# Kernel optimization log

Hardware: AMD Instinct MI355X
Metric: run time of the kernel (lower is better)

The kernel has to match this reference:

```python
import jax, jax.numpy as jnp
import numpy as np

DEPTH = 3
HEADS = 8
DIM = 512
MLP = 4096
NUM_CLASS = 4
EPS = 1e-5
SCALE = (DIM // HEADS) ** -0.5


def _layernorm(x, g, b):
    mu = jnp.mean(x, axis=-1, keepdims=True)
    var = jnp.mean(jnp.square(x - mu), axis=-1, keepdims=True)
    return (x - mu) * jax.lax.rsqrt(var + EPS) * g + b


def setup_inputs() -> dict:
    key = jax.random.key(0)
    ks = jax.random.split(key, 16)
    B, N = 2, 2560
    s = 0.02
    inp = {
        "x": jax.random.normal(ks[0], (B, N, DIM), jnp.float32),
        "mask": jax.random.randint(ks[1], (B, NUM_CLASS), 0, 2, jnp.int32),
        # per-layer params stacked on leading depth axis
        "ln1_g": jnp.ones((DEPTH, DIM), jnp.float32),
        "ln1_b": jnp.zeros((DEPTH, DIM), jnp.float32),
        "qkv_w": jax.random.normal(ks[2], (DEPTH, DIM, 3 * DIM), jnp.float32) * s,  # qkv_bias=False
        "proj_w": jax.random.normal(ks[3], (DEPTH, DIM, DIM), jnp.float32) * s,
        "proj_b": jnp.zeros((DEPTH, DIM), jnp.float32),
        "ln2_g": jnp.ones((DEPTH, DIM), jnp.float32),
        "ln2_b": jnp.zeros((DEPTH, DIM), jnp.float32),
        "ffn_w1": jax.random.normal(ks[4], (DEPTH, DIM, MLP), jnp.float32) * s,
        "ffn_b1": jnp.zeros((DEPTH, MLP), jnp.float32),
        "ffn_w2": jax.random.normal(ks[5], (DEPTH, MLP, DIM), jnp.float32) * s,
        "ffn_b2": jnp.zeros((DEPTH, DIM), jnp.float32),
    }
    return inp


def reference(x, mask, ln1_g, ln1_b, qkv_w, proj_w, proj_b, ln2_g, ln2_b,
              ffn_w1, ffn_b1, ffn_w2, ffn_b2):
    B, N, C = x.shape
    n = N // (NUM_CLASS + 1)  # tokens per modality block
    # mask_gen_fusion: columns of missing-modality blocks are masked out;
    # fusion block (last n tokens) is always attendable.
    avail = jnp.concatenate(
        [jnp.repeat(mask.astype(bool), n, axis=1), jnp.ones((B, n), bool)], axis=1)  # [B, N]
    neg_inf = jnp.asarray(-jnp.inf, x.dtype)

    attn_list = []
    for j in range(DEPTH):
        # --- masked attention block (Residual(PreNormDrop(MaskedAttention))) ---
        h = _layernorm(x, ln1_g[j], ln1_b[j])
        qkv = (h @ qkv_w[j]).reshape(B, N, 3, HEADS, C // HEADS)
        q, k, v = (qkv[:, :, i].transpose(0, 2, 1, 3) for i in range(3))  # [B,H,N,hd]
        attn = jnp.einsum("bhqd,bhkd->bhqk", q, k) * SCALE
        attn = jnp.where(avail[:, None, None, :], attn, neg_inf)
        attn = jax.nn.softmax(attn, axis=-1)
        o = jnp.einsum("bhqk,bhkd->bhqd", attn, v).transpose(0, 2, 1, 3).reshape(B, N, C)
        x = x + (o @ proj_w[j] + proj_b[j])  # dropout = identity (eval)
        attn_list.append(attn)
        # --- FFN block (Residual(PreNorm(FeedForward))) ---
        h = _layernorm(x, ln2_g[j], ln2_b[j])
        h = jax.nn.gelu(h @ ffn_w1[j] + ffn_b1[j]) @ ffn_w2[j] + ffn_b2[j]
        x = x + h
    return x, jnp.stack(attn_list, axis=0)  # [depth,B,H,N,N]
```

## Files before the change

kernel.cpp:

```cpp
#include <hip/hip_runtime.h>
#include <math.h>

#define DEPTH 3
#define HEADS 8
#define DIM 512
#define NCLS 4
#define EPSV 1e-5f
#define BB 2
#define NN 2560
#define HD 64
#define ATT_SCALE 0.125f

typedef __attribute__((ext_vector_type(8))) short bf16x8;
typedef __attribute__((ext_vector_type(4))) float f32x4;

__device__ inline unsigned short bf16_rne(float f) {
    unsigned int u = __float_as_uint(f);
    u += 0x7FFFu + ((u >> 16) & 1u);
    return (unsigned short)(u >> 16);
}
__device__ inline float bf16_tof(unsigned short h) {
    return __uint_as_float(((unsigned int)h) << 16);
}
__device__ inline void split2(float f, unsigned short& hi, unsigned short& lo) {
    hi = bf16_rne(f);
    lo = bf16_rne(f - bf16_tof(hi));
}

__device__ inline float gelu_tanh(float x) {
    float x3 = x * x * x;
    return 0.5f * x * (1.f + tanhf(0.7978845608028654f * (x + 0.044715f * x3)));
}

__device__ inline void gll16(const void* g, void* l) {
    __builtin_amdgcn_global_load_lds(
        (const __attribute__((address_space(1))) void*)g,
        (__attribute__((address_space(3))) void*)l,
        16, 0, 0);
}

template<int ROWS>
__device__ inline void stage_plane(const unsigned short* gp, int ldp,
                                   unsigned short* ls, int lane, int wave) {
#pragma unroll
    for (int q = 0; q < ROWS / 64; ++q) {
        int base = wave * (ROWS * 16) + q * 1024;
        int lpos = base + lane * 16;
        int row  = lpos >> 6;
        int ke   = (lpos & 63) >> 1;
        gll16(gp + (size_t)row * ldp + ke, (char*)ls + base);
    }
}

__device__ inline void stage_a_f32(const float* ga, int lda,
                                   unsigned short* lhi, unsigned short* llo, int tid) {
    int row = tid >> 1, half = tid & 1;
    const float* src = ga + (size_t)row * lda + half * 16;
#pragma unroll
    for (int c2 = 0; c2 < 2; ++c2) {
        float4 p0 = *(const float4*)(src + c2 * 8);
        float4 p1 = *(const float4*)(src + c2 * 8 + 4);
        float v[8] = {p0.x, p0.y, p0.z, p0.w, p1.x, p1.y, p1.z, p1.w};
        bf16x8 hv, lv;
#pragma unroll
        for (int i = 0; i < 8; ++i) {
            unsigned short h, l;
            split2(v[i], h, l);
            hv[i] = (short)h; lv[i] = (short)l;
        }
        int idx = row * 32 + (half * 2 + c2) * 8;
        *(bf16x8*)&lhi[idx] = hv;
        *(bf16x8*)&llo[idx] = lv;
    }
}

template<int BN, bool A_F32, bool DO_GELU, bool DO_RESID, bool SPLIT_OUT>
__global__ __launch_bounds__(256, 2) void gemm_mfma(
    const float* __restrict__ Af,
    const unsigned short* __restrict__ A_hi, const unsigned short* __restrict__ A_lo,
    int lda, long long sAb, long long sAh,
    const unsigned short* __restrict__ B_hi, const unsigned short* __restrict__ B_lo,
    int ldb, long long sBb, long long sBh,
    float* __restrict__ Cf,
    unsigned short* __restrict__ C_hi, unsigned short* __restrict__ C_lo,
    int ldc, long long sCb, long long sCh,
    int K, float alpha, const float* __restrict__ bias, int nh)
{
    constexpr int BM = 128;
    constexpr int WAVES_N = (BN == 128) ? 2 : 1;
    constexpr int WM = (WAVES_N == 2) ? 64 : 32;
    constexpr int WN = 64;
    constexpr int MF = WM / 16;
    constexpr int NF = WN / 16;

    __shared__ unsigned short As_hi[BM * 32], As_lo[BM * 32];
    __shared__ unsigned short Bs_hi[BN * 32], Bs_lo[BN * 32];

    const int bz = blockIdx.z / nh, hz = blockIdx.z % nh;
    const long long aoff = (long long)bz * sAb + (long long)hz * sAh;
    const long long boff = (long long)bz * sBb + (long long)hz * sBh;
    const long long coff = (long long)bz * sCb + (long long)hz * sCh;
    if (A_F32) { Af += aoff; } else { A_hi += aoff; A_lo += aoff; }
    B_hi += boff; B_lo += boff;
    if (SPLIT_OUT) { C_hi += coff; C_lo += coff; } else { Cf += coff; }

    const int tid  = threadIdx.x;
    const int lane = tid & 63;
    const int wave = tid >> 6;
    const int row0 = blockIdx.y * BM;
    const int n0   = blockIdx.x * BN;
    const int wr = (WAVES_N == 2) ? (wave >> 1) : wave;
    const int wc = (WAVES_N == 2) ? (wave & 1) : 0;
    const int lr = lane & 15;
    const int cg = lane >> 4;

    f32x4 acc[MF][NF];
#pragma unroll
    for (int m = 0; m < MF; ++m)
#pragma unroll
        for (int n = 0; n < NF; ++n)
#pragma unroll
            for (int i = 0; i < 4; ++i) acc[m][n][i] = 0.f;

    for (int k0 = 0; k0 < K; k0 += 32) {
        if constexpr (A_F32) {
            stage_a_f32(Af + (size_t)row0 * lda + k0, lda, As_hi, As_lo, tid);
        } else {
            stage_plane<BM>(A_hi + (size_t)row0 * lda + k0, lda, As_hi, lane, wave);
            stage_plane<BM>(A_lo + (size_t)row0 * lda + k0, lda, As_lo, lane, wave);
        }
        stage_plane<BN>(B_hi + (size_t)n0 * ldb + k0, ldb, Bs_hi, lane, wave);
        stage_plane<BN>(B_lo + (size_t)n0 * ldb + k0, ldb, Bs_lo, lane, wave);
        __syncthreads();

        bf16x8 ah[MF], al[MF], bh[NF], bl[NF];
#pragma unroll
        for (int m = 0; m < MF; ++m) {
            int idx = (wr * WM + m * 16 + lr) * 32 + cg * 8;
            ah[m] = *(const bf16x8*)&As_hi[idx];
            al[m] = *(const bf16x8*)&As_lo[idx];
        }
#pragma unroll
        for (int n = 0; n < NF; ++n) {
            int idx = (wc * WN + n * 16 + lr) * 32 + cg * 8;
            bh[n] = *(const bf16x8*)&Bs_hi[idx];
            bl[n] = *(const bf16x8*)&Bs_lo[idx];
        }
#pragma unroll
        for (int m = 0; m < MF; ++m)
#pragma unroll
            for (int n = 0; n < NF; ++n) {
                acc[m][n] = __builtin_amdgcn_mfma_f32_16x16x32_bf16(ah[m], bh[n], acc[m][n], 0, 0, 0);
                acc[m][n] = __builtin_amdgcn_mfma_f32_16x16x32_bf16(ah[m], bl[n], acc[m][n], 0, 0, 0);
                acc[m][n] = __builtin_amdgcn_mfma_f32_16x16x32_bf16(al[m], bh[n], acc[m][n], 0, 0, 0);
            }
        __syncthreads();
    }

    float bv[NF];
#pragma unroll
    for (int n = 0; n < NF; ++n) {
        int col = n0 + wc * WN + n * 16 + lr;
        bv[n] = bias ? bias[col] : 0.f;
    }
#pragma unroll
    for (int m = 0; m < MF; ++m) {
#pragma unroll
        for (int n = 0; n < NF; ++n) {
            int col = n0 + wc * WN + n * 16 + lr;
#pragma unroll
            for (int i = 0; i < 4; ++i) {
                int row = row0 + wr * WM + m * 16 + cg * 4 + i;
                size_t off = (size_t)row * ldc + col;
                float r = alpha * acc[m][n][i] + bv[n];
                if constexpr (DO_GELU) r = gelu_tanh(r);
                if constexpr (SPLIT_OUT) {
                    unsigned short h, l;
                    split2(r, h, l);
                    C_hi[off] = h; C_lo[off] = l;
                } else {
                    if constexpr (DO_RESID) r += Cf[off];
                    Cf[off] = r;
                }
            }
        }
    }
}

__global__ __launch_bounds__(256) void ln_split_kernel(const float* __restrict__ x,
                                                       const float* __restrict__ g,
                                                       const float* __restrict__ b,
                                                       unsigned short* __restrict__ ohi,
                                                       unsigned short* __restrict__ olo) {
    int wave = threadIdx.x >> 6;
    int lane = threadIdx.x & 63;
    int row  = blockIdx.x * 4 + wave;
    const float* xr = x + (size_t)row * DIM;
    float v[8];
    float s = 0.f, ss = 0.f;
#pragma unroll
    for (int i = 0; i < 8; ++i) {
        v[i] = xr[lane + i * 64];
        s += v[i]; ss += v[i] * v[i];
    }
#pragma unroll
    for (int off = 32; off >= 1; off >>= 1) {
        s  += __shfl_xor(s,  off, 64);
        ss += __shfl_xor(ss, off, 64);
    }
    float mu   = s * (1.f / DIM);
    float var  = ss * (1.f / DIM) - mu * mu;
    float rstd = rsqrtf(var + EPSV);
    size_t base = (size_t)row * DIM;
#pragma unroll
    for (int i = 0; i < 8; ++i) {
        int c = lane + i * 64;
        float r = (v[i] - mu) * rstd * g[c] + b[c];
        unsigned short h, l;
        split2(r, h, l);
        ohi[base + c] = h; olo[base + c] = l;
    }
}

__global__ __launch_bounds__(256) void tsplit_kernel(
    const float* __restrict__ in, int ldin, long long inBS,
    unsigned short* __restrict__ ohi, unsigned short* __restrict__ olo,
    int ldout, long long outBS) {
    __shared__ float tile[32][33];
    const float* src = in + (size_t)blockIdx.z * inBS;
    int r0 = blockIdx.y * 32, c0 = blockIdx.x * 32;
    int t = threadIdx.x;
    int r = t >> 3, cq = (t & 7) * 4;
    float4 v = *(const float4*)&src[(size_t)(r0 + r) * ldin + c0 + cq];
    tile[r][cq] = v.x; tile[r][cq + 1] = v.y; tile[r][cq + 2] = v.z; tile[r][cq + 3] = v.w;
    __syncthreads();
    unsigned short h[4], l[4];
#pragma unroll
    for (int i = 0; i < 4; ++i) split2(tile[cq + i][r], h[i], l[i]);
    size_t off = (size_t)blockIdx.z * outBS + (size_t)(c0 + r) * ldout + r0 + cq;
    *(ushort4*)&ohi[off] = make_ushort4(h[0], h[1], h[2], h[3]);
    *(ushort4*)&olo[off] = make_ushort4(l[0], l[1], l[2], l[3]);
}

__global__ __launch_bounds__(256) void softmax_kernel(float* __restrict__ attn,
                                                      const int* __restrict__ mask) {
    int q = blockIdx.x, h = blockIdx.y, b = blockIdx.z;
    float* row = attn + (((size_t)(b * HEADS + h)) * NN + q) * NN;
    int t = threadIdx.x;

    float v[10];
    bool ok[10];
    float lmax = -INFINITY;
#pragma unroll
    for (int i = 0; i < 10; ++i) {
        int col = t + i * 256;
        int cls = col >> 9;
        ok[i] = (cls >= NCLS) || (mask[b * NCLS + cls] != 0);
        v[i] = row[col];
        if (ok[i]) lmax = fmaxf(lmax, v[i]);
    }
    __shared__ float red[4];
#pragma unroll
    for (int off = 32; off >= 1; off >>= 1) lmax = fmaxf(lmax, __shfl_xor(lmax, off, 64));
    if ((t & 63) == 0) red[t >> 6] = lmax;
    __syncthreads();
    float m = fmaxf(fmaxf(red[0], red[1]), fmaxf(red[2], red[3]));
    __syncthreads();

    float lsum = 0.f;
#pragma unroll
    for (int i = 0; i < 10; ++i) {
        if (ok[i]) { v[i] = __expf(v[i] - m); lsum += v[i]; }
    }
#pragma unroll
    for (int off = 32; off >= 1; off >>= 1) lsum += __shfl_xor(lsum, off, 64);
    if ((t & 63) == 0) red[t >> 6] = lsum;
    __syncthreads();
    float inv = 1.f / (red[0] + red[1] + red[2] + red[3]);

#pragma unroll
    for (int i = 0; i < 10; ++i) {
        int col = t + i * 256;
        row[col] = ok[i] ? v[i] * inv : 0.f;
    }
}

extern "C" void kernel_launch(void* const* d_in, const int* in_sizes, int n_in,
                              void* d_out, int out_size, void* d_ws, size_t ws_size,
                              hipStream_t stream) {
    (void)in_sizes; (void)n_in; (void)out_size; (void)ws_size;
    const float* x_in   = (const float*)d_in[0];
    const int*   mask   = (const int*)d_in[1];
    const float* ln1_g  = (const float*)d_in[2];
    const float* ln1_b  = (const float*)d_in[3];
    const float* qkv_w  = (const float*)d_in[4];
    const float* proj_w = (const float*)d_in[5];
    const float* proj_b = (const float*)d_in[6];
    const float* ln2_g  = (const float*)d_in[7];
    const float* ln2_b  = (const float*)d_in[8];
    const float* ffn_w1 = (const float*)d_in[9];
    const float* ffn_b1 = (const float*)d_in[10];
    const float* ffn_w2 = (const float*)d_in[11];
    const float* ffn_b2 = (const float*)d_in[12];

    const size_t xsz = (size_t)BB * NN * DIM;
    float* xbuf     = (float*)d_out;
    float* attn_all = (float*)d_out + xsz;

    unsigned short* Wq_hi = (unsigned short*)d_ws;
    unsigned short* Wq_lo = Wq_hi + (size_t)1536 * 512;
    unsigned short* Wp_hi = Wq_lo + (size_t)1536 * 512;
    unsigned short* Wp_lo = Wp_hi + (size_t)512 * 512;
    unsigned short* W1_hi = Wp_lo + (size_t)512 * 512;
    unsigned short* W1_lo = W1_hi + (size_t)4096 * 512;
    unsigned short* W2_hi = W1_lo + (size_t)4096 * 512;
    unsigned short* W2_lo = W2_hi + (size_t)4096 * 512;
    unsigned short* h_hi  = W2_lo + (size_t)4096 * 512;
    unsigned short* h_lo  = h_hi + xsz;
    unsigned short* U     = h_lo + xsz;
    unsigned short* qk_hi = U;
    unsigned short* qk_lo = qk_hi + (size_t)5120 * 1024;
    float*          Vf    = (float*)(qk_lo + (size_t)5120 * 1024);
    unsigned short* vt_hi = (unsigned short*)(Vf + xsz);
    unsigned short* vt_lo = vt_hi + (size_t)2 * 512 * 2560;
    unsigned short* o_hi  = vt_lo + (size_t)2 * 512 * 2560;
    unsigned short* o_lo  = o_hi + xsz;
    unsigned short* g_hi  = U;
    unsigned short* g_lo  = g_hi + (size_t)5120 * 4096;

    hipMemcpyAsync(xbuf, x_in, xsz * sizeof(float), hipMemcpyDeviceToDevice, stream);

    dim3 blk(256);
    const int M = BB * NN;

    for (int j = 0; j < DEPTH; ++j) {
        tsplit_kernel<<<dim3(1536 / 32, 512 / 32, 1), blk, 0, stream>>>(
            qkv_w + (size_t)j * 512 * 1536, 1536, 0, Wq_hi, Wq_lo, 512, 0);
        tsplit_kernel<<<dim3(512 / 32, 512 / 32, 1), blk, 0, stream>>>(
            proj_w + (size_t)j * 512 * 512, 512, 0, Wp_hi, Wp_lo, 512, 0);
        tsplit_kernel<<<dim3(4096 / 32, 512 / 32, 1), blk, 0, stream>>>(
            ffn_w1 + (size_t)j * 512 * 4096, 4096, 0, W1_hi, W1_lo, 512, 0);
        tsplit_kernel<<<dim3(512 / 32, 4096 / 32, 1), blk, 0, stream>>>(
            ffn_w2 + (size_t)j * 4096 * 512, 512, 0, W2_hi, W2_lo, 4096, 0);

        ln_split_kernel<<<dim3(M / 4), blk, 0, stream>>>(xbuf, ln1_g + j * DIM, ln1_b + j * DIM, h_hi, h_lo);

        gemm_mfma<128, false, false, false, true><<<dim3(8, 40, 1), blk, 0, stream>>>(
            nullptr, h_hi, h_lo, DIM, 0, 0,
            Wq_hi, Wq_lo, DIM, 0, 0,
            nullptr, qk_hi, qk_lo, 1024, 0, 0,
            DIM, 1.f, nullptr, 1);
        gemm_mfma<128, false, false, false, false><<<dim3(4, 40, 1), blk, 0, stream>>>(
            nullptr, h_hi, h_lo, DIM, 0, 0,
            Wq_hi + (size_t)1024 * 512, Wq_lo + (size_t)1024 * 512, DIM, 0, 0,
            Vf, nullptr, nullptr, DIM, 0, 0,
            DIM, 1.f, nullptr, 1);
        tsplit_kernel<<<dim3(512 / 32, 2560 / 32, BB), blk, 0, stream>>>(
            Vf, DIM, (long long)NN * DIM, vt_hi, vt_lo, NN, (long long)DIM * NN);

        float* attn_j = attn_all + (size_t)j * BB * HEADS * NN * NN;
        gemm_mfma<128, false, false, false, false><<<dim3(20, 20, BB * HEADS), blk, 0, stream>>>(
            nullptr, qk_hi, qk_lo, 1024, (long long)NN * 1024, HD,
            qk_hi + 512, qk_lo + 512, 1024, (long long)NN * 1024, HD,
            attn_j, nullptr, nullptr, NN, (long long)HEADS * NN * NN, (long long)NN * NN,
            HD, ATT_SCALE, nullptr, HEADS);

        softmax_kernel<<<dim3(NN, HEADS, BB), blk, 0, stream>>>(attn_j, mask);

        gemm_mfma<64, true, false, false, true><<<dim3(1, 20, BB * HEADS), blk, 0, stream>>>(
            attn_j, nullptr, nullptr, NN, (long long)HEADS * NN * NN, (long long)NN * NN,
            vt_hi, vt_lo, NN, (long long)DIM * NN, (long long)HD * NN,
            nullptr, o_hi, o_lo, DIM, (long long)NN * DIM, HD,
            NN, 1.f, nullptr, HEADS);

        gemm_mfma<128, false, false, true, false><<<dim3(4, 40, 1), blk, 0, stream>>>(
            nullptr, o_hi, o_lo, DIM, 0, 0,
            Wp_hi, Wp_lo, DIM, 0, 0,
            xbuf, nullptr, nullptr, DIM, 0, 0,
            DIM, 1.f, proj_b + j * DIM, 1);

        ln_split_kernel<<<dim3(M / 4), blk, 0, stream>>>(xbuf, ln2_g + j * DIM, ln2_b + j * DIM, h_hi, h_lo);

        gemm_mfma<128, false, true, false, true><<<dim3(32, 40, 1), blk, 0, stream>>>(
            nullptr, h_hi, h_lo, DIM, 0, 0,
            W1_hi, W1_lo, DIM, 0, 0,
            nullptr, g_hi, g_lo, 4096, 0, 0,
            DIM, 1.f, ffn_b1 + (size_t)j * 4096, 1);

        gemm_mfma<128, false, false, true, false><<<dim3(4, 40, 1), blk, 0, stream>>>(
            nullptr, g_hi, g_lo, 4096, 0, 0,
            W2_hi, W2_lo, 4096, 0, 0,
            xbuf, nullptr, nullptr, DIM, 0, 0,
            4096, 1.f, ffn_b2 + j * DIM, 1);
    }
}
```

Baseline: 3.614 ms.

## Swizzle LDS layout, remap blocks across XCDs, and shrink N-tiles for narrow GEMMs

XOR-swizzles the 16-byte chunks in the LDS tiles on both the global-to-LDS stage and the fragment reads, to cut LDS bank conflicts. Adds a block-index remap so consecutive flat block IDs are spread across the 8 XCD partitions. Switches the narrow N=512 GEMMs (V, proj, FFN2) to 64-wide tiles, doubling their grid, and raises launch_bounds occupancy for BN=64. The remap adds integer divides and relies on the total block count being divisible by 8.

Result: faster. 3.229 ms (-10.7%).

```diff
diff --git a/kernel.cpp b/kernel.cpp
--- a/kernel.cpp
+++ b/kernel.cpp
@@ -32,6 +32,8 @@
     return 0.5f * x * (1.f + tanhf(0.7978845608028654f * (x + 0.044715f * x3)));
 }
 
+__device__ inline int swz(int row, int chunk) { return chunk ^ ((row >> 1) & 3); }
+
 __device__ inline void gll16(const void* g, void* l) {
     __builtin_amdgcn_global_load_lds(
         (const __attribute__((address_space(1))) void*)g,
@@ -47,8 +49,9 @@
         int base = wave * (ROWS * 16) + q * 1024;
         int lpos = base + lane * 16;
         int row  = lpos >> 6;
-        int ke   = (lpos & 63) >> 1;
-        gll16(gp + (size_t)row * ldp + ke, (char*)ls + base);
+        int cl   = (lpos >> 4) & 3;
+        int cg   = swz(row, cl);
+        gll16(gp + (size_t)row * ldp + cg * 8, (char*)ls + base);
     }
 }
 
@@ -68,14 +71,15 @@
             split2(v[i], h, l);
             hv[i] = (short)h; lv[i] = (short)l;
         }
-        int idx = row * 32 + (half * 2 + c2) * 8;
+        int chunk = half * 2 + c2;
+        int idx = row * 32 + swz(row, chunk) * 8;
         *(bf16x8*)&lhi[idx] = hv;
         *(bf16x8*)&llo[idx] = lv;
     }
 }
 
-template<int BN, bool A_F32, bool DO_GELU, bool DO_RESID, bool SPLIT_OUT>
-__global__ __launch_bounds__(256, 2) void gemm_mfma(
+template<int BN, bool A_F32, bool DO_GELU, bool DO_RESID, bool SPLIT_OUT, bool ZSWZ>
+__global__ __launch_bounds__(256, (BN == 128 ? 2 : 3)) void gemm_mfma(
     const float* __restrict__ Af,
     const unsigned short* __restrict__ A_hi, const unsigned short* __restrict__ A_lo,
     int lda, long long sAb, long long sAh,
@@ -96,7 +100,21 @@
     __shared__ unsigned short As_hi[BM * 32], As_lo[BM * 32];
     __shared__ unsigned short Bs_hi[BN * 32], Bs_lo[BN * 32];
 
-    const int bz = blockIdx.z / nh, hz = blockIdx.z % nh;
+    int bx = blockIdx.x, by = blockIdx.y, bzz = blockIdx.z;
+    if constexpr (ZSWZ) {
+        int gx = gridDim.x, gy = gridDim.y, gz = gridDim.z;
+        int pb = gx * gy;
+        int total = pb * gz;
+        int flat = bx + gx * (by + gy * bzz);
+        int cpx = total >> 3;
+        int nf = (flat & 7) * cpx + (flat >> 3);
+        bzz = nf / pb;
+        int r = nf - bzz * pb;
+        by = r / gx;
+        bx = r - by * gx;
+    }
+
+    const int bz = bzz / nh, hz = bzz % nh;
     const long long aoff = (long long)bz * sAb + (long long)hz * sAh;
     const long long boff = (long long)bz * sBb + (long long)hz * sBh;
     const long long coff = (long long)bz * sCb + (long long)hz * sCh;
@@ -107,8 +125,8 @@
     const int tid  = threadIdx.x;
     const int lane = tid & 63;
     const int wave = tid >> 6;
-    const int row0 = blockIdx.y * BM;
-    const int n0   = blockIdx.x * BN;
+    const int row0 = by * BM;
+    const int n0   = bx * BN;
     const int wr = (WAVES_N == 2) ? (wave >> 1) : wave;
     const int wc = (WAVES_N == 2) ? (wave & 1) : 0;
     const int lr = lane & 15;
@@ -136,13 +154,15 @@
         bf16x8 ah[MF], al[MF], bh[NF], bl[NF];
 #pragma unroll
         for (int m = 0; m < MF; ++m) {
-            int idx = (wr * WM + m * 16 + lr) * 32 + cg * 8;
+            int r = wr * WM + m * 16 + lr;
+            int idx = r * 32 + swz(r, cg) * 8;
             ah[m] = *(const bf16x8*)&As_hi[idx];
             al[m] = *(const bf16x8*)&As_lo[idx];
         }
 #pragma unroll
         for (int n = 0; n < NF; ++n) {
-            int idx = (wc * WN + n * 16 + lr) * 32 + cg * 8;
+            int r = wc * WN + n * 16 + lr;
+            int idx = r * 32 + swz(r, cg) * 8;
             bh[n] = *(const bf16x8*)&Bs_hi[idx];
             bl[n] = *(const bf16x8*)&Bs_lo[idx];
         }
@@ -345,12 +365,12 @@
 
         ln_split_kernel<<<dim3(M / 4), blk, 0, stream>>>(xbuf, ln1_g + j * DIM, ln1_b + j * DIM, h_hi, h_lo);
 
-        gemm_mfma<128, false, false, false, true><<<dim3(8, 40, 1), blk, 0, stream>>>(
+        gemm_mfma<128, false, false, false, true, true><<<dim3(8, 40, 1), blk, 0, stream>>>(
             nullptr, h_hi, h_lo, DIM, 0, 0,
             Wq_hi, Wq_lo, DIM, 0, 0,
             nullptr, qk_hi, qk_lo, 1024, 0, 0,
             DIM, 1.f, nullptr, 1);
-        gemm_mfma<128, false, false, false, false><<<dim3(4, 40, 1), blk, 0, stream>>>(
+        gemm_mfma<64, false, false, false, false, true><<<dim3(8, 40, 1), blk, 0, stream>>>(
             nullptr, h_hi, h_lo, DIM, 0, 0,
             Wq_hi + (size_t)1024 * 512, Wq_lo + (size_t)1024 * 512, DIM, 0, 0,
             Vf, nullptr, nullptr, DIM, 0, 0,
@@ -359,7 +379,7 @@
             Vf, DIM, (long long)NN * DIM, vt_hi, vt_lo, NN, (long long)DIM * NN);
 
         float* attn_j = attn_all + (size_t)j * BB * HEADS * NN * NN;
-        gemm_mfma<128, false, false, false, false><<<dim3(20, 20, BB * HEADS), blk, 0, stream>>>(
+        gemm_mfma<128, false, false, false, false, true><<<dim3(20, 20, BB * HEADS), blk, 0, stream>>>(
             nullptr, qk_hi, qk_lo, 1024, (long long)NN * 1024, HD,
             qk_hi + 512, qk_lo + 512, 1024, (long long)NN * 1024, HD,
             attn_j, nullptr, nullptr, NN, (long long)HEADS * NN * NN, (long long)NN * NN,
@@ -367,13 +387,13 @@
 
         softmax_kernel<<<dim3(NN, HEADS, BB), blk, 0, stream>>>(attn_j, mask);
 
-        gemm_mfma<64, true, false, false, true><<<dim3(1, 20, BB * HEADS), blk, 0, stream>>>(
+        gemm_mfma<64, true, false, false, true, true><<<dim3(1, 20, BB * HEADS), blk, 0, stream>>>(
             attn_j, nullptr, nullptr, NN, (long long)HEADS * NN * NN, (long long)NN * NN,
             vt_hi, vt_lo, NN, (long long)DIM * NN, (long long)HD * NN,
             nullptr, o_hi, o_lo, DIM, (long long)NN * DIM, HD,
             NN, 1.f, nullptr, HEADS);
 
-        gemm_mfma<128, false, false, true, false><<<dim3(4, 40, 1), blk, 0, stream>>>(
+        gemm_mfma<64, false, false, true, false, true><<<dim3(8, 40, 1), blk, 0, stream>>>(
             nullptr, o_hi, o_lo, DIM, 0, 0,
             Wp_hi, Wp_lo, DIM, 0, 0,
             xbuf, nullptr, nullptr, DIM, 0, 0,
@@ -381,13 +401,13 @@
 
         ln_split_kernel<<<dim3(M / 4), blk, 0, stream>>>(xbuf, ln2_g + j * DIM, ln2_b + j * DIM, h_hi, h_lo);
 
-        gemm_mfma<128, false, true, false, true><<<dim3(32, 40, 1), blk, 0, stream>>>(
+        gemm_mfma<128, false, true, false, true, true><<<dim3(32, 40, 1), blk, 0, stream>>>(
             nullptr, h_hi, h_lo, DIM, 0, 0,
             W1_hi, W1_lo, DIM, 0, 0,
             nullptr, g_hi, g_lo, 4096, 0, 0,
             DIM, 1.f, ffn_b1 + (size_t)j * 4096, 1);
 
-        gemm_mfma<128, false, false, true, false><<<dim3(4, 40, 1), blk, 0, stream>>>(
+        gemm_mfma<64, false, false, true, false, true><<<dim3(8, 40, 1), blk, 0, stream>>>(
             nullptr, g_hi, g_lo, 4096, 0, 0,
             W2_hi, W2_lo, 4096, 0, 0,
             xbuf, nullptr, nullptr, DIM, 0, 0,
```
